# Optimization experiments

Measured on AMD Instinct MI355X. Metric: run time of the kernel, lower is better.

The kernel has to match this reference:

```python
import jax, jax.numpy as jnp
import numpy as np

N = 100000   # nodes
E = 1600000  # edges
F_IN = 128
H = 128      # hidden_channels
G = 1000     # graphs in batch
EPS = 1e-5


def setup_inputs() -> dict:
    key = jax.random.key(0)
    ks = jax.random.split(key, 20)
    x = jax.random.normal(ks[0], (N, F_IN), dtype=jnp.float32)
    edge_index = jax.random.randint(ks[1], (2, E), 0, N, dtype=jnp.int64)
    batch = jnp.sort(jax.random.randint(ks[2], (N,), 0, G, dtype=jnp.int64))
    s = 0.05
    inp = {
        "x": x,
        "edge_index": edge_index,
        "batch": batch,
        "W1": jax.random.normal(ks[3], (F_IN, H), dtype=jnp.float32) * s,
        "b1": jnp.zeros((H,), jnp.float32),
        "g1": jnp.ones((H,), jnp.float32),
        "be1": jnp.zeros((H,), jnp.float32),
        "W2": jax.random.normal(ks[4], (H, H), dtype=jnp.float32) * s,
        "b2": jnp.zeros((H,), jnp.float32),
        "g2": jnp.ones((H,), jnp.float32),
        "be2": jnp.zeros((H,), jnp.float32),
        "W3": jax.random.normal(ks[5], (H, H), dtype=jnp.float32) * s,
        "b3": jnp.zeros((H,), jnp.float32),
        "g3": jnp.ones((H,), jnp.float32),
        "be3": jnp.zeros((H,), jnp.float32),
        "Wl": jax.random.normal(ks[6], (H, 1), dtype=jnp.float32) * s,
        "bl": jnp.zeros((1,), jnp.float32),
    }
    return inp


def _gcn_conv(x, W, b, src, dst, dinv):
    # PyG GCNConv: h = x W; out[d] = sum_e dinv[src]*dinv[dst]*h[src]; out += b
    h = x @ W
    coef = (dinv[src] * dinv[dst])[:, None]
    msg = h[src] * coef                       # [E+N, H] gather + scale
    out = jax.ops.segment_sum(msg, dst, num_segments=N)
    return out + b


def _bn_relu(x, g, be):
    # BatchNorm1d training mode: batch stats, biased variance
    m = jnp.mean(x, axis=0)
    v = jnp.var(x, axis=0)
    xn = (x - m) * jax.lax.rsqrt(v + EPS)
    return jax.nn.relu(xn * g + be)


def reference(x, edge_index, batch, W1, b1, g1, be1, W2, b2, g2, be2,
              W3, b3, g3, be3, Wl, bl):
    loop = jnp.arange(N, dtype=edge_index.dtype)
    src = jnp.concatenate([edge_index[0], loop])  # self-loops appended
    dst = jnp.concatenate([edge_index[1], loop])
    deg = jax.ops.segment_sum(jnp.ones_like(dst, dtype=x.dtype), dst,
                              num_segments=N)
    dinv = jax.lax.rsqrt(deg)                     # deg >= 1 (self-loops)

    h = _bn_relu(_gcn_conv(x, W1, b1, src, dst, dinv), g1, be1)
    h = _bn_relu(_gcn_conv(h, W2, b2, src, dst, dinv), g2, be2)
    h = _bn_relu(_gcn_conv(h, W3, b3, src, dst, dinv), g3, be3)

    # global_mean_pool over graph ids
    sums = jax.ops.segment_sum(h, batch, num_segments=G)
    cnt = jax.ops.segment_sum(jnp.ones((N,), h.dtype), batch, num_segments=G)
    pooled = sums / jnp.maximum(cnt, 1.0)[:, None]

    return pooled @ Wl + bl
```

## Files before the change

kernel.cpp:

```cpp
#include <hip/hip_runtime.h>
#include <hip/hip_bf16.h>

#define Nn 100000
#define Ee 1600000
#define Hh 128
#define Gg 1000
#define EPSb 1e-5f

#define SCAN_CHUNK 1024
#define NB_SCAN 98
#define AGG_BLOCKS 2048
#define GEMM_BLOCKS 782

typedef unsigned int uint;
typedef short short8 __attribute__((ext_vector_type(8)));
typedef float floatx4 __attribute__((ext_vector_type(4)));

static __device__ __forceinline__ uint bf16rne(float f) {
    uint u = __float_as_uint(f);
    return (u + 0x7fffu + ((u >> 16) & 1u)) >> 16;
}
static __device__ __forceinline__ float bflo(uint u) { return __uint_as_float(u << 16); }
static __device__ __forceinline__ float bfhi(uint u) { return __uint_as_float(u & 0xffff0000u); }


__global__ void k_init(int* __restrict__ deg, int* __restrict__ cursor,
                       float* __restrict__ colsum) {
    int i = blockIdx.x * blockDim.x + threadIdx.x;
    if (i < Nn) { deg[i] = 1; cursor[i] = 0; }
    if (i < 256) colsum[i] = 0.f;
}

__global__ void k_deg(const int* __restrict__ dst, int* __restrict__ deg) {
    int i = blockIdx.x * blockDim.x + threadIdx.x;
    if (i < Ee) atomicAdd(&deg[dst[i]], 1);
}

__global__ void k_dinv(const int* __restrict__ deg, float* __restrict__ dinv) {
    int i = blockIdx.x * blockDim.x + threadIdx.x;
    if (i < Nn) dinv[i] = rsqrtf((float)deg[i]);
}

__global__ void k_scan1(const int* __restrict__ deg, int* __restrict__ bsum) {
    __shared__ int ls[256];
    int t = threadIdx.x;
    int base = blockIdx.x * SCAN_CHUNK + t * 4;
    int s = 0;
#pragma unroll
    for (int j = 0; j < 4; ++j) { int i = base + j; if (i < Nn) s += deg[i]; }
    ls[t] = s;
    __syncthreads();
    for (int off = 128; off; off >>= 1) {
        if (t < off) ls[t] += ls[t + off];
        __syncthreads();
    }
    if (t == 0) bsum[blockIdx.x] = ls[0];
}

__global__ void k_scan2(int* __restrict__ bsum, int nb) {
    int acc = 0;
    for (int b = 0; b < nb; ++b) { int v = bsum[b]; bsum[b] = acc; acc += v; }
}

__global__ void k_scan3(const int* __restrict__ deg, const int* __restrict__ bsum,
                        int* __restrict__ offs) {
    __shared__ int ls[256];
    int t = threadIdx.x;
    int base = blockIdx.x * SCAN_CHUNK + t * 4;
    int d[4]; int s = 0;
#pragma unroll
    for (int j = 0; j < 4; ++j) {
        int i = base + j;
        d[j] = (i < Nn) ? deg[i] : 0;
        s += d[j];
    }
    ls[t] = s;
    __syncthreads();
    for (int off = 1; off < 256; off <<= 1) {
        int u = (t >= off) ? ls[t - off] : 0;
        __syncthreads();
        ls[t] += u;
        __syncthreads();
    }
    int run = bsum[blockIdx.x] + ls[t] - s;
#pragma unroll
    for (int j = 0; j < 4; ++j) {
        int i = base + j;
        if (i < Nn) offs[i] = run;
        run += d[j];
    }
    if (blockIdx.x == 0 && t == 0) offs[Nn] = Ee + Nn;
}

__global__ void k_fill(const int* __restrict__ src, const int* __restrict__ dst,
                       const int* __restrict__ offs, int* __restrict__ cursor,
                       const float* __restrict__ dinv,
                       int2* __restrict__ adj) {
    int i = blockIdx.x * blockDim.x + threadIdx.x;
    if (i >= Ee + Nn) return;
    int s, d;
    if (i < Ee) { s = src[i]; d = dst[i]; }
    else        { s = d = i - Ee; }
    int pos = offs[d] + atomicAdd(&cursor[d], 1);
    adj[pos] = make_int2(s, __float_as_int(dinv[s] * dinv[d]));
}


__global__ void k_wconv(const float* __restrict__ W, uint* __restrict__ Wtp) {
    int idx = blockIdx.x * blockDim.x + threadIdx.x;
    if (idx >= 128 * 64) return;
    int n = idx >> 6, ku = idx & 63;
    uint lo = bf16rne(W[(size_t)(2 * ku) * 128 + n]);
    uint hi = bf16rne(W[(size_t)(2 * ku + 1) * 128 + n]);
    Wtp[(size_t)n * 64 + ku] = lo | (hi << 16);
}


__global__ __launch_bounds__(256) void k_gemm(
    const float* __restrict__ inf, const uint* __restrict__ inb,
    const uint* __restrict__ Wtp,
    const float* __restrict__ scale, const float* __restrict__ shift,
    uint* __restrict__ outb, int mode) {
    __shared__ uint XT[128][64];
    __shared__ uint WT[128][64];
    int t = threadIdx.x;
    int rowBase = blockIdx.x * 128;
    int r = t >> 1, half = t & 1;

    {
        int gr = rowBase + r;
        int grc = gr < Nn ? gr : Nn - 1;
        if (mode == 0) {
            const float* sp = inf + (size_t)grc * 128 + half * 64;
#pragma unroll
            for (int q = 0; q < 8; ++q) {
                float4 v0 = *(const float4*)(sp + q * 8);
                float4 v1 = *(const float4*)(sp + q * 8 + 4);
                uint4 o;
                o.x = bf16rne(v0.x) | (bf16rne(v0.y) << 16);
                o.y = bf16rne(v0.z) | (bf16rne(v0.w) << 16);
                o.z = bf16rne(v1.x) | (bf16rne(v1.y) << 16);
                o.w = bf16rne(v1.z) | (bf16rne(v1.w) << 16);
                int g = half * 8 + q;
                *(uint4*)&XT[r][(g ^ (r & 7)) << 2] = o;
            }
        } else {
            const uint* sp = inb + (size_t)grc * 64 + half * 32;
#pragma unroll
            for (int q = 0; q < 8; ++q) {
                uint4 v = *(const uint4*)(sp + q * 4);
                int fb = half * 64 + q * 8;
                float4 s0 = *(const float4*)(scale + fb);
                float4 s1 = *(const float4*)(scale + fb + 4);
                float4 h0 = *(const float4*)(shift + fb);
                float4 h1 = *(const float4*)(shift + fb + 4);
                float a0 = fmaxf(fmaf(bflo(v.x), s0.x, h0.x), 0.f);
                float a1 = fmaxf(fmaf(bfhi(v.x), s0.y, h0.y), 0.f);
                float a2 = fmaxf(fmaf(bflo(v.y), s0.z, h0.z), 0.f);
                float a3 = fmaxf(fmaf(bfhi(v.y), s0.w, h0.w), 0.f);
                float a4 = fmaxf(fmaf(bflo(v.z), s1.x, h1.x), 0.f);
                float a5 = fmaxf(fmaf(bfhi(v.z), s1.y, h1.y), 0.f);
                float a6 = fmaxf(fmaf(bflo(v.w), s1.z, h1.z), 0.f);
                float a7 = fmaxf(fmaf(bfhi(v.w), s1.w, h1.w), 0.f);
                uint4 o;
                o.x = bf16rne(a0) | (bf16rne(a1) << 16);
                o.y = bf16rne(a2) | (bf16rne(a3) << 16);
                o.z = bf16rne(a4) | (bf16rne(a5) << 16);
                o.w = bf16rne(a6) | (bf16rne(a7) << 16);
                int g = half * 8 + q;
                *(uint4*)&XT[r][(g ^ (r & 7)) << 2] = o;
            }
        }
    }
    {
        const uint* sp = Wtp + (size_t)r * 64 + half * 32;
#pragma unroll
        for (int q = 0; q < 8; ++q) {
            uint4 v = *(const uint4*)(sp + q * 4);
            int g = half * 8 + q;
            *(uint4*)&WT[r][(g ^ (r & 7)) << 2] = v;
        }
    }
    __syncthreads();

    int l = t & 63, w = t >> 6;
    int nb = (w >> 1) * 64;
    int fb2 = (w & 1) * 64;
    int lr = l & 15, lk = l >> 4;
    floatx4 zero = {0.f, 0.f, 0.f, 0.f};
    floatx4 acc[4][4];
#pragma unroll
    for (int mi = 0; mi < 4; ++mi)
#pragma unroll
        for (int ni = 0; ni < 4; ++ni) acc[mi][ni] = zero;

#pragma unroll
    for (int kc = 0; kc < 4; ++kc) {
        short8 xf[4], wf[4];
        int g = kc * 4 + lk;
#pragma unroll
        for (int mi = 0; mi < 4; ++mi) {
            int rr = nb + mi * 16 + lr;
            xf[mi] = *(const short8*)&XT[rr][(g ^ (rr & 7)) << 2];
        }
#pragma unroll
        for (int ni = 0; ni < 4; ++ni) {
            int rr = fb2 + ni * 16 + lr;
            wf[ni] = *(const short8*)&WT[rr][(g ^ (rr & 7)) << 2];
        }
#pragma unroll
        for (int mi = 0; mi < 4; ++mi)
#pragma unroll
            for (int ni = 0; ni < 4; ++ni)
                acc[mi][ni] = __builtin_amdgcn_mfma_f32_16x16x32_bf16(
                    wf[ni], xf[mi], acc[mi][ni], 0, 0, 0);
    }

#pragma unroll
    for (int mi = 0; mi < 4; ++mi) {
        int node = rowBase + nb + mi * 16 + lr;
        if (node < Nn) {
            uint* op = outb + (size_t)node * 64;
#pragma unroll
            for (int ni = 0; ni < 4; ++ni) {
                int fo = fb2 + ni * 16 + lk * 4;
                uint2 o;
                o.x = bf16rne(acc[mi][ni][0]) | (bf16rne(acc[mi][ni][1]) << 16);
                o.y = bf16rne(acc[mi][ni][2]) | (bf16rne(acc[mi][ni][3]) << 16);
                *(uint2*)(op + (fo >> 1)) = o;
            }
        }
    }
}


__global__ __launch_bounds__(256) void k_agg(
    const uint* __restrict__ h32, const int* __restrict__ offs,
    const int2* __restrict__ adj,
    const float* __restrict__ bias, uint* __restrict__ agg,
    float* __restrict__ colsum) {
    __shared__ float ls[256];
    int tid = threadIdx.x;
    ls[tid] = 0.f;
    __syncthreads();
    int lane = tid & 63;
    int gw = blockIdx.x * 4 + (tid >> 6);
    int nw = gridDim.x * 4;
    int c0 = lane * 2;
    float b0 = bias[c0], b1 = bias[c0 + 1];
    float ps0 = 0.f, pq0 = 0.f, ps1 = 0.f, pq1 = 0.f;
    for (int d = gw; d < Nn; d += nw) {
        int beg = offs[d], end = offs[d + 1];
        float a0 = 0.f, a1 = 0.f;
        int i = beg;
        for (; i + 8 <= end; i += 8) {
            int2 e[8];
#pragma unroll
            for (int j = 0; j < 8; ++j) e[j] = adj[i + j];
            uint hv[8];
#pragma unroll
            for (int j = 0; j < 8; ++j)
                hv[j] = h32[(size_t)e[j].x * 64 + lane];
#pragma unroll
            for (int j = 0; j < 8; ++j) {
                float w = __int_as_float(e[j].y);
                a0 = fmaf(w, bflo(hv[j]), a0);
                a1 = fmaf(w, bfhi(hv[j]), a1);
            }
        }
        for (; i < end; ++i) {
            int2 e = adj[i];
            uint hv = h32[(size_t)e.x * 64 + lane];
            float w = __int_as_float(e.y);
            a0 = fmaf(w, bflo(hv), a0);
            a1 = fmaf(w, bfhi(hv), a1);
        }
        a0 += b0; a1 += b1;
        agg[(size_t)d * 64 + lane] = bf16rne(a0) | (bf16rne(a1) << 16);
        ps0 += a0; pq0 += a0 * a0;
        ps1 += a1; pq1 += a1 * a1;
    }
    atomicAdd(&ls[c0], ps0);
    atomicAdd(&ls[c0 + 1], ps1);
    atomicAdd(&ls[128 + c0], pq0);
    atomicAdd(&ls[128 + c0 + 1], pq1);
    __syncthreads();
    atomicAdd(&colsum[tid], ls[tid]);
}


__global__ void k_bnfinal(float* __restrict__ colsum,
                          const float* __restrict__ g, const float* __restrict__ be,
                          float* __restrict__ scale, float* __restrict__ shift) {
    int t = threadIdx.x;
    float s = colsum[t], q = colsum[128 + t];
    float m = s * (1.0f / Nn);
    float var = q * (1.0f / Nn) - m * m;
    float istd = rsqrtf(var + EPSb);
    float sc = istd * g[t];
    scale[t] = sc;
    shift[t] = fmaf(-m, sc, be[t]);
    colsum[t] = 0.f;
    colsum[128 + t] = 0.f;
}


__global__ __launch_bounds__(256) void k_pool(
    const uint* __restrict__ agg, const int* __restrict__ batch,
    const float* __restrict__ scale, const float* __restrict__ shift,
    const float* __restrict__ Wl, const float* __restrict__ bl,
    float* __restrict__ out) {
    int lane = threadIdx.x & 63;
    int g = (blockIdx.x * blockDim.x + threadIdx.x) >> 6;
    if (g >= Gg) return;
    int lo = 0, hi = Nn;
    while (lo < hi) { int mid = (lo + hi) >> 1; if (batch[mid] < g) lo = mid + 1; else hi = mid; }
    int beg = lo;
    hi = Nn;
    while (lo < hi) { int mid = (lo + hi) >> 1; if (batch[mid] < g + 1) lo = mid + 1; else hi = mid; }
    int end = lo;
    int c0 = lane * 2;
    float sc0 = scale[c0], sh0 = shift[c0];
    float sc1 = scale[c0 + 1], sh1 = shift[c0 + 1];
    float s0 = 0.f, s1 = 0.f;
    for (int n = beg; n < end; ++n) {
        uint v = agg[(size_t)n * 64 + lane];
        s0 += fmaxf(fmaf(bflo(v), sc0, sh0), 0.f);
        s1 += fmaxf(fmaf(bfhi(v), sc1, sh1), 0.f);
    }
    float inv = 1.0f / fmaxf((float)(end - beg), 1.0f);
    float part = (s0 * inv) * Wl[c0] + (s1 * inv) * Wl[c0 + 1];
#pragma unroll
    for (int off = 32; off; off >>= 1) part += __shfl_down(part, off);
    if (lane == 0) out[g] = part + bl[0];
}


extern "C" void kernel_launch(void* const* d_in, const int* in_sizes, int n_in,
                              void* d_out, int out_size, void* d_ws, size_t ws_size,
                              hipStream_t stream) {
    const float* x   = (const float*)d_in[0];
    const int*   ei  = (const int*)d_in[1];
    const int*   src = ei;
    const int*   dst = ei + Ee;
    const int*   bat = (const int*)d_in[2];
    const float* W1 = (const float*)d_in[3];
    const float* b1 = (const float*)d_in[4];
    const float* g1 = (const float*)d_in[5];
    const float* be1 = (const float*)d_in[6];
    const float* W2 = (const float*)d_in[7];
    const float* b2 = (const float*)d_in[8];
    const float* g2 = (const float*)d_in[9];
    const float* be2 = (const float*)d_in[10];
    const float* W3 = (const float*)d_in[11];
    const float* b3 = (const float*)d_in[12];
    const float* g3 = (const float*)d_in[13];
    const float* be3 = (const float*)d_in[14];
    const float* Wl = (const float*)d_in[15];
    const float* bl = (const float*)d_in[16];
    float* out = (float*)d_out;

    char* w = (char*)d_ws;
    auto alloc = [&](size_t bytes) {
        void* p = (void*)w;
        w += (bytes + 255) & ~(size_t)255;
        return p;
    };
    int*   deg    = (int*)alloc((size_t)Nn * 4);
    int*   cursor = (int*)alloc((size_t)Nn * 4);
    int*   offs   = (int*)alloc((size_t)(Nn + 1) * 4);
    int*   bsum   = (int*)alloc(256 * 4);
    float* dinv   = (float*)alloc((size_t)Nn * 4);
    float* colsum = (float*)alloc(256 * 4);
    float* scale  = (float*)alloc(128 * 4);
    float* shift  = (float*)alloc(128 * 4);
    uint*  Wt1    = (uint*)alloc(128 * 64 * 4);
    uint*  Wt2    = (uint*)alloc(128 * 64 * 4);
    uint*  Wt3    = (uint*)alloc(128 * 64 * 4);
    int2*  adj    = (int2*)alloc((size_t)(Ee + Nn) * 8);
    uint*  tmp    = (uint*)alloc((size_t)Nn * 64 * 4);
    uint*  agg    = (uint*)alloc((size_t)Nn * 64 * 4);

    k_init<<<(Nn + 255) / 256, 256, 0, stream>>>(deg, cursor, colsum);
    k_deg<<<(Ee + 255) / 256, 256, 0, stream>>>(dst, deg);
    k_dinv<<<(Nn + 255) / 256, 256, 0, stream>>>(deg, dinv);
    k_scan1<<<NB_SCAN, 256, 0, stream>>>(deg, bsum);
    k_scan2<<<1, 1, 0, stream>>>(bsum, NB_SCAN);
    k_scan3<<<NB_SCAN, 256, 0, stream>>>(deg, bsum, offs);
    k_fill<<<(Ee + Nn + 255) / 256, 256, 0, stream>>>(src, dst, offs, cursor, dinv, adj);
    k_wconv<<<32, 256, 0, stream>>>(W1, Wt1);
    k_wconv<<<32, 256, 0, stream>>>(W2, Wt2);
    k_wconv<<<32, 256, 0, stream>>>(W3, Wt3);
    k_gemm<<<GEMM_BLOCKS, 256, 0, stream>>>(x, (const uint*)0, Wt1, scale, shift, tmp, 0);
    k_agg<<<AGG_BLOCKS, 256, 0, stream>>>(tmp, offs, adj, b1, agg, colsum);
    k_bnfinal<<<1, 128, 0, stream>>>(colsum, g1, be1, scale, shift);
    k_gemm<<<GEMM_BLOCKS, 256, 0, stream>>>((const float*)0, agg, Wt2, scale, shift, tmp, 1);
    k_agg<<<AGG_BLOCKS, 256, 0, stream>>>(tmp, offs, adj, b2, agg, colsum);
    k_bnfinal<<<1, 128, 0, stream>>>(colsum, g2, be2, scale, shift);
    k_gemm<<<GEMM_BLOCKS, 256, 0, stream>>>((const float*)0, agg, Wt3, scale, shift, tmp, 1);
    k_agg<<<AGG_BLOCKS, 256, 0, stream>>>(tmp, offs, adj, b3, agg, colsum);
    k_bnfinal<<<1, 128, 0, stream>>>(colsum, g3, be3, scale, shift);
    k_pool<<<(Gg * 64 + 255) / 256, 256, 0, stream>>>(agg, bat, scale, shift, Wl, bl, out);
}
```

Baseline: 623.4 us.

## Store hidden features in 16-column slices and aggregate per slice with edge-parallel lanes

Hidden activations move from row-major [N,128] bf16 to eight feature-sliced planes of 16 columns each, and the GEMM, aggregation and pooling kernels are rewritten to match. In aggregation, each block now serves one slice, and each wave handles 8 edges at once, with 8 lanes covering the 16 columns; partial sums are then combined with xor shuffles. The aim is a smaller gather footprint per slice and more memory-level parallelism on short adjacency lists. The cost is that every edge list is read once per slice (8 times in total), and a cross-lane reduction is added for each node.

```diff
diff --git a/kernel.cpp b/kernel.cpp
--- a/kernel.cpp
+++ b/kernel.cpp
@@ -13,6 +13,7 @@
 #define GEMM_BLOCKS 782
 
 typedef unsigned int uint;
+typedef unsigned long long u64;
 typedef short short8 __attribute__((ext_vector_type(8)));
 typedef float floatx4 __attribute__((ext_vector_type(4)));
 
@@ -22,6 +23,7 @@
 }
 static __device__ __forceinline__ float bflo(uint u) { return __uint_as_float(u << 16); }
 static __device__ __forceinline__ float bfhi(uint u) { return __uint_as_float(u & 0xffff0000u); }
+
 
 
 __global__ void k_init(int* __restrict__ deg, int* __restrict__ cursor,
@@ -145,10 +147,10 @@
                 *(uint4*)&XT[r][(g ^ (r & 7)) << 2] = o;
             }
         } else {
-            const uint* sp = inb + (size_t)grc * 64 + half * 32;
 #pragma unroll
             for (int q = 0; q < 8; ++q) {
-                uint4 v = *(const uint4*)(sp + q * 4);
+                int sl = half * 4 + (q >> 1);
+                uint4 v = *(const uint4*)(inb + ((size_t)sl * Nn + grc) * 8 + (q & 1) * 4);
                 int fb = half * 64 + q * 8;
                 float4 s0 = *(const float4*)(scale + fb);
                 float4 s1 = *(const float4*)(scale + fb + 4);
@@ -220,14 +222,13 @@
     for (int mi = 0; mi < 4; ++mi) {
         int node = rowBase + nb + mi * 16 + lr;
         if (node < Nn) {
-            uint* op = outb + (size_t)node * 64;
 #pragma unroll
             for (int ni = 0; ni < 4; ++ni) {
-                int fo = fb2 + ni * 16 + lk * 4;
+                int slice = (fb2 >> 4) + ni;
                 uint2 o;
                 o.x = bf16rne(acc[mi][ni][0]) | (bf16rne(acc[mi][ni][1]) << 16);
                 o.y = bf16rne(acc[mi][ni][2]) | (bf16rne(acc[mi][ni][3]) << 16);
-                *(uint2*)(op + (fo >> 1)) = o;
+                *(uint2*)(outb + ((size_t)slice * Nn + node) * 8 + lk * 2) = o;
             }
         }
     }
@@ -235,57 +236,69 @@
 
 
 __global__ __launch_bounds__(256) void k_agg(
-    const uint* __restrict__ h32, const int* __restrict__ offs,
+    const uint* __restrict__ hs, const int* __restrict__ offs,
     const int2* __restrict__ adj,
-    const float* __restrict__ bias, uint* __restrict__ agg,
+    const float* __restrict__ bias, uint* __restrict__ aggs,
     float* __restrict__ colsum) {
-    __shared__ float ls[256];
+    __shared__ float ls[32];
     int tid = threadIdx.x;
-    ls[tid] = 0.f;
+    if (tid < 32) ls[tid] = 0.f;
     __syncthreads();
+    int s = blockIdx.x & 7;
+    int nb = blockIdx.x >> 3;
+    int wv = tid >> 6;
     int lane = tid & 63;
-    int gw = blockIdx.x * 4 + (tid >> 6);
-    int nw = gridDim.x * 4;
-    int c0 = lane * 2;
-    float b0 = bias[c0], b1 = bias[c0 + 1];
-    float ps0 = 0.f, pq0 = 0.f, ps1 = 0.f, pq1 = 0.f;
-    for (int d = gw; d < Nn; d += nw) {
+    int grp = lane >> 3;
+    int col = lane & 7;
+    int f0 = s * 16 + col * 2;
+    float b0 = bias[f0], b1 = bias[f0 + 1];
+    const uint* hbase = hs + (size_t)s * Nn * 8;
+    uint* abase = aggs + (size_t)s * Nn * 8;
+    const u64* adj8 = (const u64*)adj;
+    float ps0 = 0.f, ps1 = 0.f, pq0 = 0.f, pq1 = 0.f;
+    for (int d = nb * 4 + wv; d < Nn; d += 1024) {
         int beg = offs[d], end = offs[d + 1];
         float a0 = 0.f, a1 = 0.f;
-        int i = beg;
-        for (; i + 8 <= end; i += 8) {
-            int2 e[8];
-#pragma unroll
-            for (int j = 0; j < 8; ++j) e[j] = adj[i + j];
-            uint hv[8];
-#pragma unroll
-            for (int j = 0; j < 8; ++j)
-                hv[j] = h32[(size_t)e[j].x * 64 + lane];
-#pragma unroll
-            for (int j = 0; j < 8; ++j) {
-                float w = __int_as_float(e[j].y);
-                a0 = fmaf(w, bflo(hv[j]), a0);
-                a1 = fmaf(w, bfhi(hv[j]), a1);
-            }
-        }
-        for (; i < end; ++i) {
-            int2 e = adj[i];
-            uint hv = h32[(size_t)e.x * 64 + lane];
-            float w = __int_as_float(e.y);
+        int nfull = (end - beg) & ~7;
+        int iend = beg + nfull;
+        for (int i = beg; i < iend; i += 8) {
+            u64 e = __builtin_nontemporal_load(&adj8[i + grp]);
+            int src = (int)(e & 0xffffffffu);
+            float w = __uint_as_float((uint)(e >> 32));
+            uint hv = hbase[(size_t)src * 8 + col];
             a0 = fmaf(w, bflo(hv), a0);
             a1 = fmaf(w, bfhi(hv), a1);
         }
+        int i = iend + grp;
+        if (i < end) {
+            u64 e = __builtin_nontemporal_load(&adj8[i]);
+            int src = (int)(e & 0xffffffffu);
+            float w = __uint_as_float((uint)(e >> 32));
+            uint hv = hbase[(size_t)src * 8 + col];
+            a0 = fmaf(w, bflo(hv), a0);
+            a1 = fmaf(w, bfhi(hv), a1);
+        }
+#pragma unroll
+        for (int m = 8; m < 64; m <<= 1) {
+            a0 += __shfl_xor(a0, m);
+            a1 += __shfl_xor(a1, m);
+        }
         a0 += b0; a1 += b1;
-        agg[(size_t)d * 64 + lane] = bf16rne(a0) | (bf16rne(a1) << 16);
-        ps0 += a0; pq0 += a0 * a0;
-        ps1 += a1; pq1 += a1 * a1;
-    }
-    atomicAdd(&ls[c0], ps0);
-    atomicAdd(&ls[c0 + 1], ps1);
-    atomicAdd(&ls[128 + c0], pq0);
-    atomicAdd(&ls[128 + c0 + 1], pq1);
+        if (grp == 0) {
+            abase[(size_t)d * 8 + col] = bf16rne(a0) | (bf16rne(a1) << 16);
+            ps0 += a0; pq0 += a0 * a0;
+            ps1 += a1; pq1 += a1 * a1;
+        }
+    }
+    if (grp == 0) {
+        atomicAdd(&ls[col * 2], ps0);
+        atomicAdd(&ls[col * 2 + 1], ps1);
+        atomicAdd(&ls[16 + col * 2], pq0);
+        atomicAdd(&ls[16 + col * 2 + 1], pq1);
+    }
     __syncthreads();
-    atomicAdd(&colsum[tid], ls[tid]);
+    if (tid < 16)      atomicAdd(&colsum[s * 16 + tid], ls[tid]);
+    else if (tid < 32) atomicAdd(&colsum[128 + s * 16 + (tid - 16)], ls[tid]);
 }
 
 
@@ -319,12 +332,14 @@
     hi = Nn;
     while (lo < hi) { int mid = (lo + hi) >> 1; if (batch[mid] < g + 1) lo = mid + 1; else hi = mid; }
     int end = lo;
-    int c0 = lane * 2;
+    int sl = lane >> 3, j = lane & 7;
+    int c0 = sl * 16 + j * 2;
+    const uint* base = agg + (size_t)sl * Nn * 8 + j;
     float sc0 = scale[c0], sh0 = shift[c0];
     float sc1 = scale[c0 + 1], sh1 = shift[c0 + 1];
     float s0 = 0.f, s1 = 0.f;
     for (int n = beg; n < end; ++n) {
-        uint v = agg[(size_t)n * 64 + lane];
+        uint v = base[(size_t)n * 8];
         s0 += fmaxf(fmaf(bflo(v), sc0, sh0), 0.f);
         s1 += fmaxf(fmaf(bfhi(v), sc1, sh1), 0.f);
     }
```

Result: slower. 1.077 ms (+72.8%).

## Fold BN finalize into consumers, merge small setup kernels, pipeline agg loads

Applied to the files above, without the earlier changes.

Removes the k_bnfinal, k_dinv and per-layer weight-conversion launches. BN scale/shift are now computed per block inside the next GEMM and inside pool, using a separate column-sum buffer per layer, and dinv is written by the scan kernel. The aggregation loop software-pipelines the adjacency loads one chunk ahead and splits the accumulation into two chains to expose more memory parallelism. Every GEMM block redoes the small BN finalize, and the pipelined loop uses more registers.

```diff
diff --git a/kernel.cpp b/kernel.cpp
--- a/kernel.cpp
+++ b/kernel.cpp
@@ -28,17 +28,12 @@
                        float* __restrict__ colsum) {
     int i = blockIdx.x * blockDim.x + threadIdx.x;
     if (i < Nn) { deg[i] = 1; cursor[i] = 0; }
-    if (i < 256) colsum[i] = 0.f;
+    if (i < 768) colsum[i] = 0.f;
 }
 
 __global__ void k_deg(const int* __restrict__ dst, int* __restrict__ deg) {
     int i = blockIdx.x * blockDim.x + threadIdx.x;
     if (i < Ee) atomicAdd(&deg[dst[i]], 1);
-}
-
-__global__ void k_dinv(const int* __restrict__ deg, float* __restrict__ dinv) {
-    int i = blockIdx.x * blockDim.x + threadIdx.x;
-    if (i < Nn) dinv[i] = rsqrtf((float)deg[i]);
 }
 
 __global__ void k_scan1(const int* __restrict__ deg, int* __restrict__ bsum) {
@@ -63,7 +58,7 @@
 }
 
 __global__ void k_scan3(const int* __restrict__ deg, const int* __restrict__ bsum,
-                        int* __restrict__ offs) {
+                        int* __restrict__ offs, float* __restrict__ dinv) {
     __shared__ int ls[256];
     int t = threadIdx.x;
     int base = blockIdx.x * SCAN_CHUNK + t * 4;
@@ -86,7 +81,10 @@
 #pragma unroll
     for (int j = 0; j < 4; ++j) {
         int i = base + j;
-        if (i < Nn) offs[i] = run;
+        if (i < Nn) {
+            offs[i] = run;
+            dinv[i] = rsqrtf((float)d[j]);
+        }
         run += d[j];
     }
     if (blockIdx.x == 0 && t == 0) offs[Nn] = Ee + Nn;
@@ -106,26 +104,44 @@
 }
 
 
-__global__ void k_wconv(const float* __restrict__ W, uint* __restrict__ Wtp) {
+__global__ void k_wconv3(const float* __restrict__ W1, const float* __restrict__ W2,
+                         const float* __restrict__ W3, uint* __restrict__ Wt) {
     int idx = blockIdx.x * blockDim.x + threadIdx.x;
-    if (idx >= 128 * 64) return;
-    int n = idx >> 6, ku = idx & 63;
+    if (idx >= 3 * 8192) return;
+    const float* W = (idx < 8192) ? W1 : ((idx < 16384) ? W2 : W3);
+    int k = idx & 8191;
+    int n = k >> 6, ku = k & 63;
     uint lo = bf16rne(W[(size_t)(2 * ku) * 128 + n]);
     uint hi = bf16rne(W[(size_t)(2 * ku + 1) * 128 + n]);
-    Wtp[(size_t)n * 64 + ku] = lo | (hi << 16);
+    Wt[(size_t)(idx >> 13) * 8192 + n * 64 + ku] = lo | (hi << 16);
 }
 
 
 __global__ __launch_bounds__(256) void k_gemm(
     const float* __restrict__ inf, const uint* __restrict__ inb,
     const uint* __restrict__ Wtp,
-    const float* __restrict__ scale, const float* __restrict__ shift,
+    const float* __restrict__ cs, const float* __restrict__ gg,
+    const float* __restrict__ be,
     uint* __restrict__ outb, int mode) {
     __shared__ uint XT[128][64];
     __shared__ uint WT[128][64];
+    __shared__ float scsh[256];
     int t = threadIdx.x;
     int rowBase = blockIdx.x * 128;
     int r = t >> 1, half = t & 1;
+
+    if (mode) {
+        if (t < 128) {
+            float s = cs[t], q = cs[128 + t];
+            float m = s * (1.0f / Nn);
+            float var = q * (1.0f / Nn) - m * m;
+            float istd = rsqrtf(var + EPSb);
+            float sc = istd * gg[t];
+            scsh[t] = sc;
+            scsh[128 + t] = fmaf(-m, sc, be[t]);
+        }
+        __syncthreads();
+    }
 
     {
         int gr = rowBase + r;
@@ -150,25 +166,20 @@
             for (int q = 0; q < 8; ++q) {
                 uint4 v = *(const uint4*)(sp + q * 4);
                 int fb = half * 64 + q * 8;
-                float4 s0 = *(const float4*)(scale + fb);
-                float4 s1 = *(const float4*)(scale + fb + 4);
-                float4 h0 = *(const float4*)(shift + fb);
-                float4 h1 = *(const float4*)(shift + fb + 4);
-                float a0 = fmaxf(fmaf(bflo(v.x), s0.x, h0.x), 0.f);
-                float a1 = fmaxf(fmaf(bfhi(v.x), s0.y, h0.y), 0.f);
-                float a2 = fmaxf(fmaf(bflo(v.y), s0.z, h0.z), 0.f);
-                float a3 = fmaxf(fmaf(bfhi(v.y), s0.w, h0.w), 0.f);
-                float a4 = fmaxf(fmaf(bflo(v.z), s1.x, h1.x), 0.f);
-                float a5 = fmaxf(fmaf(bfhi(v.z), s1.y, h1.y), 0.f);
-                float a6 = fmaxf(fmaf(bflo(v.w), s1.z, h1.z), 0.f);
-                float a7 = fmaxf(fmaf(bfhi(v.w), s1.w, h1.w), 0.f);
-                uint4 o;
-                o.x = bf16rne(a0) | (bf16rne(a1) << 16);
-                o.y = bf16rne(a2) | (bf16rne(a3) << 16);
-                o.z = bf16rne(a4) | (bf16rne(a5) << 16);
-                o.w = bf16rne(a6) | (bf16rne(a7) << 16);
+                float av[8] = {bflo(v.x), bfhi(v.x), bflo(v.y), bfhi(v.y),
+                               bflo(v.z), bfhi(v.z), bflo(v.w), bfhi(v.w)};
+                uint o[4];
+#pragma unroll
+                for (int k2 = 0; k2 < 4; ++k2) {
+                    float lo = fmaxf(fmaf(av[2 * k2], scsh[fb + 2 * k2],
+                                          scsh[128 + fb + 2 * k2]), 0.f);
+                    float hi = fmaxf(fmaf(av[2 * k2 + 1], scsh[fb + 2 * k2 + 1],
+                                          scsh[128 + fb + 2 * k2 + 1]), 0.f);
+                    o[k2] = bf16rne(lo) | (bf16rne(hi) << 16);
+                }
+                uint4 ov = make_uint4(o[0], o[1], o[2], o[3]);
                 int g = half * 8 + q;
-                *(uint4*)&XT[r][(g ^ (r & 7)) << 2] = o;
+                *(uint4*)&XT[r][(g ^ (r & 7)) << 2] = ov;
             }
         }
     }
@@ -245,27 +256,61 @@
     __syncthreads();
     int lane = tid & 63;
     int gw = blockIdx.x * 4 + (tid >> 6);
-    int nw = gridDim.x * 4;
+    int nw = AGG_BLOCKS * 4;
     int c0 = lane * 2;
-    float b0 = bias[c0], b1 = bias[c0 + 1];
+    float bb0 = bias[c0], bb1 = bias[c0 + 1];
     float ps0 = 0.f, pq0 = 0.f, ps1 = 0.f, pq1 = 0.f;
     for (int d = gw; d < Nn; d += nw) {
         int beg = offs[d], end = offs[d + 1];
-        float a0 = 0.f, a1 = 0.f;
+        float a0 = 0.f, a1 = 0.f, x0 = 0.f, x1 = 0.f;
         int i = beg;
-        for (; i + 8 <= end; i += 8) {
+        int nch = (end - beg) >> 3;
+        if (nch > 0) {
             int2 e[8];
 #pragma unroll
             for (int j = 0; j < 8; ++j) e[j] = adj[i + j];
-            uint hv[8];
-#pragma unroll
-            for (int j = 0; j < 8; ++j)
-                hv[j] = h32[(size_t)e[j].x * 64 + lane];
-#pragma unroll
-            for (int j = 0; j < 8; ++j) {
-                float w = __int_as_float(e[j].y);
-                a0 = fmaf(w, bflo(hv[j]), a0);
-                a1 = fmaf(w, bfhi(hv[j]), a1);
+            for (int ch = 1; ch < nch; ++ch) {
+                uint hv[8];
+#pragma unroll
+                for (int j = 0; j < 8; ++j)
+                    hv[j] = h32[(size_t)e[j].x * 64 + lane];
+                int2 en[8];
+#pragma unroll
+                for (int j = 0; j < 8; ++j) en[j] = adj[i + 8 + j];
+#pragma unroll
+                for (int j = 0; j < 4; ++j) {
+                    float w = __int_as_float(e[j].y);
+                    a0 = fmaf(w, bflo(hv[j]), a0);
+                    a1 = fmaf(w, bfhi(hv[j]), a1);
+                }
+#pragma unroll
+                for (int j = 4; j < 8; ++j) {
+                    float w = __int_as_float(e[j].y);
+                    x0 = fmaf(w, bflo(hv[j]), x0);
+                    x1 = fmaf(w, bfhi(hv[j]), x1);
+                }
+#pragma unroll
+                for (int j = 0; j < 8; ++j) e[j] = en[j];
+                i += 8;
+            }
+            {
+                uint hv[8];
+#pragma unroll
+                for (int j = 0; j < 8; ++j)
+                    hv[j] = h32[(size_t)e[j].x * 64 + lane];
+#pragma unroll
+                for (int j = 0; j < 4; ++j) {
+                    float w = __int_as_float(e[j].y);
+                    a0 = fmaf(w, bflo(hv[j]), a0);
+                    a1 = fmaf(w, bfhi(hv[j]), a1);
+                }
+#pragma unroll
+                for (int j = 4; j < 8; ++j) {
+                    float w = __int_as_float(e[j].y);
+                    x0 = fmaf(w, bflo(hv[j]), x0);
+                    x1 = fmaf(w, bfhi(hv[j]), x1);
+                }
+                i += 8;
             }
         }
         for (; i < end; ++i) {
@@ -275,7 +320,8 @@
             a0 = fmaf(w, bflo(hv), a0);
             a1 = fmaf(w, bfhi(hv), a1);
         }
-        a0 += b0; a1 += b1;
+        a0 += x0 + bb0;
+        a1 += x1 + bb1;
         agg[(size_t)d * 64 + lane] = bf16rne(a0) | (bf16rne(a1) << 16);
         ps0 += a0; pq0 += a0 * a0;
         ps1 += a1; pq1 += a1 * a1;
@@ -289,29 +335,26 @@
 }
 
 
-__global__ void k_bnfinal(float* __restrict__ colsum,
-                          const float* __restrict__ g, const float* __restrict__ be,
-                          float* __restrict__ scale, float* __restrict__ shift) {
-    int t = threadIdx.x;
-    float s = colsum[t], q = colsum[128 + t];
-    float m = s * (1.0f / Nn);
-    float var = q * (1.0f / Nn) - m * m;
-    float istd = rsqrtf(var + EPSb);
-    float sc = istd * g[t];
-    scale[t] = sc;
-    shift[t] = fmaf(-m, sc, be[t]);
-    colsum[t] = 0.f;
-    colsum[128 + t] = 0.f;
-}
-
-
 __global__ __launch_bounds__(256) void k_pool(
     const uint* __restrict__ agg, const int* __restrict__ batch,
-    const float* __restrict__ scale, const float* __restrict__ shift,
+    const float* __restrict__ cs, const float* __restrict__ gg,
+    const float* __restrict__ be,
     const float* __restrict__ Wl, const float* __restrict__ bl,
     float* __restrict__ out) {
-    int lane = threadIdx.x & 63;
-    int g = (blockIdx.x * blockDim.x + threadIdx.x) >> 6;
+    __shared__ float scsh[256];
+    int tid = threadIdx.x;
+    if (tid < 128) {
+        float s = cs[tid], q = cs[128 + tid];
+        float m = s * (1.0f / Nn);
+        float var = q * (1.0f / Nn) - m * m;
+        float istd = rsqrtf(var + EPSb);
+        float sc = istd * gg[tid];
+        scsh[tid] = sc;
+        scsh[128 + tid] = fmaf(-m, sc, be[tid]);
+    }
+    __syncthreads();
+    int lane = tid & 63;
+    int g = (blockIdx.x * blockDim.x + tid) >> 6;
     if (g >= Gg) return;
     int lo = 0, hi = Nn;
     while (lo < hi) { int mid = (lo + hi) >> 1; if (batch[mid] < g) lo = mid + 1; else hi = mid; }
@@ -320,8 +363,8 @@
     while (lo < hi) { int mid = (lo + hi) >> 1; if (batch[mid] < g + 1) lo = mid + 1; else hi = mid; }
     int end = lo;
     int c0 = lane * 2;
-    float sc0 = scale[c0], sh0 = shift[c0];
-    float sc1 = scale[c0 + 1], sh1 = shift[c0 + 1];
+    float sc0 = scsh[c0], sh0 = scsh[128 + c0];
+    float sc1 = scsh[c0 + 1], sh1 = scsh[128 + c0 + 1];
     float s0 = 0.f, s1 = 0.f;
     for (int n = beg; n < end; ++n) {
         uint v = agg[(size_t)n * 64 + lane];
@@ -371,34 +414,33 @@
     int*   offs   = (int*)alloc((size_t)(Nn + 1) * 4);
     int*   bsum   = (int*)alloc(256 * 4);
     float* dinv   = (float*)alloc((size_t)Nn * 4);
-    float* colsum = (float*)alloc(256 * 4);
-    float* scale  = (float*)alloc(128 * 4);
-    float* shift  = (float*)alloc(128 * 4);
-    uint*  Wt1    = (uint*)alloc(128 * 64 * 4);
-    uint*  Wt2    = (uint*)alloc(128 * 64 * 4);
-    uint*  Wt3    = (uint*)alloc(128 * 64 * 4);
+    float* colsum = (float*)alloc(768 * 4);
+    uint*  Wt     = (uint*)alloc((size_t)3 * 8192 * 4);
     int2*  adj    = (int2*)alloc((size_t)(Ee + Nn) * 8);
     uint*  tmp    = (uint*)alloc((size_t)Nn * 64 * 4);
     uint*  agg    = (uint*)alloc((size_t)Nn * 64 * 4);
 
+    float* csA = colsum;
+    float* csB = colsum + 256;
+    float* csC = colsum + 512;
+
     k_init<<<(Nn + 255) / 256, 256, 0, stream>>>(deg, cursor, colsum);
     k_deg<<<(Ee + 255) / 256, 256, 0, stream>>>(dst, deg);
-    k_dinv<<<(Nn + 255) / 256, 256, 0, stream>>>(deg, dinv);
     k_scan1<<<NB_SCAN, 256, 0, stream>>>(deg, bsum);
     k_scan2<<<1, 1, 0, stream>>>(bsum, NB_SCAN);
-    k_scan3<<<NB_SCAN, 256, 0, stream>>>(deg, bsum, offs);
+    k_scan3<<<NB_SCAN, 256, 0, stream>>>(deg, bsum, offs, dinv);
     k_fill<<<(Ee + Nn + 255) / 256, 256, 0, stream>>>(src, dst, offs, cursor, dinv, adj);
-    k_wconv<<<32, 256, 0, stream>>>(W1, Wt1);
-    k_wconv<<<32, 256, 0, stream>>>(W2, Wt2);
-    k_wconv<<<32, 256, 0, stream>>>(W3, Wt3);
-    k_gemm<<<GEMM_BLOCKS, 256, 0, stream>>>(x, (const uint*)0, Wt1, scale, shift, tmp, 0);
-    k_agg<<<AGG_BLOCKS, 256, 0, stream>>>(tmp, offs, adj, b1, agg, colsum);
-    k_bnfinal<<<1, 128, 0, stream>>>(colsum, g1, be1, scale, shift);
-    k_gemm<<<GEMM_BLOCKS, 256, 0, stream>>>((const float*)0, agg, Wt2, scale, shift, tmp, 1);
-    k_agg<<<AGG_BLOCKS, 256, 0, stream>>>(tmp, offs, adj, b2, agg, colsum);
-    k_bnfinal<<<1, 128, 0, stream>>>(colsum, g2, be2, scale, shift);
-    k_gemm<<<GEMM_BLOCKS, 256, 0, stream>>>((const float*)0, agg, Wt3, scale, shift, tmp, 1);
-    k_agg<<<AGG_BLOCKS, 256, 0, stream>>>(tmp, offs, adj, b3, agg, colsum);
-    k_bnfinal<<<1, 128, 0, stream>>>(colsum, g3, be3, scale, shift);
-    k_pool<<<(Gg * 64 + 255) / 256, 256, 0, stream>>>(agg, bat, scale, shift, Wl, bl, out);
-}
+    k_wconv3<<<96, 256, 0, stream>>>(W1, W2, W3, Wt);
+    k_gemm<<<GEMM_BLOCKS, 256, 0, stream>>>(x, (const uint*)0, Wt,
+                                            (const float*)0, (const float*)0,
+                                            (const float*)0, tmp, 0);
+    k_agg<<<AGG_BLOCKS, 256, 0, stream>>>(tmp, offs, adj, b1, agg, csA);
+    k_gemm<<<GEMM_BLOCKS, 256, 0, stream>>>((const float*)0, agg, Wt + 8192,
+                                            csA, g1, be1, tmp, 1);
+    k_agg<<<AGG_BLOCKS, 256, 0, stream>>>(tmp, offs, adj, b2, agg, csB);
+    k_gemm<<<GEMM_BLOCKS, 256, 0, stream>>>((const float*)0, agg, Wt + 16384,
+                                            csB, g2, be2, tmp, 1);
+    k_agg<<<AGG_BLOCKS, 256, 0, stream>>>(tmp, offs, adj, b3, agg, csC);
+    k_pool<<<(Gg * 64 + 255) / 256, 256, 0, stream>>>(agg, bat, csC, g3, be3,
+                                                      Wl, bl, out);
+}
```

New measurement: 682.8 us. 9.5% more time.
